# Performance work log

Hardware: AMD Instinct MI355X
Metric: run time of the kernel (lower is better)

The kernel has to match this reference:

```python
import jax, jax.numpy as jnp
import numpy as np

HEAD_DIM = 128
NUM_Q_HEADS = 32
NUM_KV_HEADS = 8
HIDDEN = HEAD_DIM * NUM_Q_HEADS  # 4096
ROPE_BASE = 10000.0


def setup_inputs() -> dict:
    key = jax.random.key(0)
    k1, k2, k3, k4, k5 = jax.random.split(key, 5)
    B, S = 1, 2048
    scale = 0.02  # keep activations sane given integer-valued x
    input_ids = jax.random.randint(k5, (B, S), 0, 100, dtype=jnp.int64) if jax.config.jax_enable_x64 else jax.random.randint(k5, (B, S), 0, 100, dtype=jnp.int32)
    position_ids = (jnp.arange(B * S).reshape(B, S) % S).astype(input_ids.dtype)
    Wq = jax.random.normal(k1, (HIDDEN, NUM_Q_HEADS * HEAD_DIM), dtype=jnp.float32) * scale
    Wk = jax.random.normal(k2, (HIDDEN, NUM_KV_HEADS * HEAD_DIM), dtype=jnp.float32) * scale
    Wv = jax.random.normal(k3, (HIDDEN, NUM_KV_HEADS * HEAD_DIM), dtype=jnp.float32) * scale
    Wo = jax.random.normal(k4, (NUM_Q_HEADS * HEAD_DIM, HIDDEN), dtype=jnp.float32) * scale
    return {"input_ids": input_ids, "position_ids": position_ids,
            "Wq": Wq, "Wk": Wk, "Wv": Wv, "Wo": Wo}


def _rotate_half(x):
    x1, x2 = jnp.split(x, 2, axis=-1)
    return jnp.concatenate([-x2, x1], axis=-1)


def _cos_sin(position_ids):
    # standard RoPE cos/sin, shape [B, S, 1, head_dim]
    inv_freq = 1.0 / (ROPE_BASE ** (jnp.arange(0, HEAD_DIM, 2, dtype=jnp.float32) / HEAD_DIM))
    ang = position_ids.astype(jnp.float32)[..., None] * inv_freq  # [B,S,d/2]
    cos = jnp.concatenate([jnp.cos(ang), jnp.cos(ang)], axis=-1)[:, :, None, :]
    sin = jnp.concatenate([jnp.sin(ang), jnp.sin(ang)], axis=-1)[:, :, None, :]
    return cos, sin


def reference(input_ids, position_ids, Wq, Wk, Wv, Wo):
    B, S = input_ids.shape
    # x = input_ids broadcast to hidden_size (as in the torch model)
    x = jnp.broadcast_to(input_ids[..., None].astype(jnp.float32), (B, S, HIDDEN))
    q = (x @ Wq).reshape(B, S, NUM_Q_HEADS, HEAD_DIM)
    k = (x @ Wk).reshape(B, S, NUM_KV_HEADS, HEAD_DIM)
    v = (x @ Wv).reshape(B, S, NUM_KV_HEADS, HEAD_DIM)
    cos, sin = _cos_sin(position_ids)
    q = q * cos + _rotate_half(q) * sin
    k = k * cos + _rotate_half(k) * sin
    # GQA: group q heads over kv heads
    G = NUM_Q_HEADS // NUM_KV_HEADS
    qg = q.reshape(B, S, NUM_KV_HEADS, G, HEAD_DIM)
    scores = jnp.einsum('bqhgd,bkhd->bhgqk', qg, k) / jnp.sqrt(jnp.float32(HEAD_DIM))
    causal = jnp.tril(jnp.ones((S, S), dtype=bool))  # [S_q, S_k]
    scores = jnp.where(causal, scores, -jnp.inf)
    attn = jax.nn.softmax(scores, axis=-1)
    out = jnp.einsum('bhgqk,bkhd->bqhgd', attn, v).reshape(B, S, NUM_Q_HEADS * HEAD_DIM)
    return out @ Wo
```

## Files before the change

### kernel.cpp

```cpp
#include <hip/hip_runtime.h>
#include <math.h>


#define HID 4096
#define NQH 32
#define NKVH 8
#define HD 128
#define CHQ 128
#define TS 64
#define RSQRT_HD 0.08838834764831845f
#define LOG2E    1.4426950408889634f

__device__ __forceinline__ void colsum_seq(const float* __restrict__ W,
                                           float* __restrict__ P,
                                           int nth4, int u) {
    const float4* b = reinterpret_cast<const float4*>(W);
    float ax = 0.f, ay = 0.f, az = 0.f, aw = 0.f;
#pragma unroll
    for (int k = 0; k < 32; k += 8) {
        float4 tt[8];
#pragma unroll
        for (int i = 0; i < 8; ++i) tt[i] = b[(size_t)(k + i) * nth4 + u];
#pragma unroll
        for (int i = 0; i < 8; i += 4) {
            ax += (tt[i].x + tt[i+1].x) + (tt[i+2].x + tt[i+3].x);
            ay += (tt[i].y + tt[i+1].y) + (tt[i+2].y + tt[i+3].y);
            az += (tt[i].z + tt[i+1].z) + (tt[i+2].z + tt[i+3].z);
            aw += (tt[i].w + tt[i+1].w) + (tt[i+2].w + tt[i+3].w);
        }
    }
    reinterpret_cast<float4*>(P)[u] = make_float4(ax, ay, az, aw);
}

__global__ __launch_bounds__(256) void k_part(
        const int* __restrict__ ids,
        const float* __restrict__ Wq, const float* __restrict__ Wk,
        const float* __restrict__ Wv,
        float* __restrict__ Pq, float* __restrict__ Pk, float* __restrict__ Pv,
        float* __restrict__ cp, double* __restrict__ Tc,
        double* __restrict__ Ts, int S) {
    int t = blockIdx.x;
    int tid = threadIdx.x;
    int nxb = S >> 8;
    int trigT = 64 * nxb;
    if (t < trigT) {
        int j = t / nxb, xb = t - j * nxb;
        int dlt = xb * 256 + tid;
        double f = (double)(float)(1.0 / pow(10000.0, (double)j / 64.0));
        double sv, cv;
        sincos((double)dlt * f, &sv, &cv);
        Tc[(size_t)j * S + dlt] = cv;
        Ts[(size_t)j * S + dlt] = sv;
        if (j == 0) cp[dlt] = (float)ids[dlt];
    } else if (t < trigT + 512) {
        colsum_seq(Wq, Pq, 512 * 256, (t - trigT) * 256 + tid);
    } else if (t < trigT + 640) {
        colsum_seq(Wk, Pk, 128 * 256, (t - trigT - 512) * 256 + tid);
    } else {
        colsum_seq(Wv, Pv, 128 * 256, (t - trigT - 640) * 256 + tid);
    }
}

__global__ __launch_bounds__(256) void k_red(
        const float* __restrict__ Pq, const float* __restrict__ Pk,
        const float* __restrict__ Pv, float* __restrict__ Sq,
        float* __restrict__ Sk, float* __restrict__ Sv) {
    int t = blockIdx.x;
    const float* P; float* Sd; int cols4, c4;
    if (t < 4)      { P = Pq; Sd = Sq; cols4 = NQH * HD / 4; c4 = t * 256 + threadIdx.x; }
    else if (t == 4){ P = Pk; Sd = Sk; cols4 = NKVH * HD / 4; c4 = threadIdx.x; }
    else            { P = Pv; Sd = Sv; cols4 = NKVH * HD / 4; c4 = threadIdx.x; }
    const float4* b = reinterpret_cast<const float4*>(P);
    float ax = 0.f, ay = 0.f, az = 0.f, aw = 0.f;
    for (int c = 0; c < CHQ; c += 16) {
        float4 tt[16];
#pragma unroll
        for (int i = 0; i < 16; ++i) tt[i] = b[(size_t)(c + i) * cols4 + c4];
#pragma unroll
        for (int i = 0; i < 16; i += 4) {
            ax += (tt[i].x + tt[i+1].x) + (tt[i+2].x + tt[i+3].x);
            ay += (tt[i].y + tt[i+1].y) + (tt[i+2].y + tt[i+3].y);
            az += (tt[i].z + tt[i+1].z) + (tt[i+2].z + tt[i+3].z);
            aw += (tt[i].w + tt[i+1].w) + (tt[i+2].w + tt[i+3].w);
        }
    }
    reinterpret_cast<float4*>(Sd)[c4] = make_float4(ax, ay, az, aw);
}

__global__ __launch_bounds__(256) void k_mid(
        const float* __restrict__ Sq, const float* __restrict__ Sk,
        const float* __restrict__ Sv, const float* __restrict__ Wo,
        const double* __restrict__ Tc, const double* __restrict__ Ts,
        float* __restrict__ Mp, float* __restrict__ D, int S) {
    int t = blockIdx.x;
    int tid = threadIdx.x;
    if (t < 512) {
        int sl = t & 3, x = (t >> 2) & 3, hg = t >> 4;
        int h = hg >> 2, dbase = hg * HD + sl * 32;
        int i4 = x * 256 + tid;
        const float4* b = reinterpret_cast<const float4*>(Wo);
        const float* sv = Sv + h * HD + sl * 32;
        float ax = 0.f, ay = 0.f, az = 0.f, aw = 0.f;
#pragma unroll
        for (int bb = 0; bb < 4; ++bb) {
            size_t p = (size_t)(dbase + bb * 8) * (HID / 4) + i4;
            float4 tt[8]; float ss[8];
#pragma unroll
            for (int i = 0; i < 8; ++i) { tt[i] = b[p + (size_t)i * (HID / 4)]; ss[i] = sv[bb * 8 + i]; }
#pragma unroll
            for (int i = 0; i < 8; ++i) {
                ax += ss[i] * tt[i].x; ay += ss[i] * tt[i].y;
                az += ss[i] * tt[i].z; aw += ss[i] * tt[i].w;
            }
        }
        reinterpret_cast<float4*>(Mp)[((size_t)sl * NQH + hg) * (HID / 4) + i4] =
            make_float4(ax, ay, az, aw);
    } else {
        __shared__ double p[64], q[64];
        int u = t - 512;
        int nxb = S >> 8;
        int hg = u / nxb, xb = u - hg * nxb, h = hg >> 2;
        if (tid < 64) {
            double a1 = Sq[hg * HD + tid], a2 = Sq[hg * HD + tid + 64];
            double b1 = Sk[h * HD + tid],  b2 = Sk[h * HD + tid + 64];
            p[tid] = a1 * b1 + a2 * b2;
            q[tid] = a2 * b1 - a1 * b2;
        }
        __syncthreads();
        int dlt = xb * 256 + tid;
        const double* tc = Tc + dlt;
        const double* ts = Ts + dlt;
        double acc = 0.0;
#pragma unroll 8
        for (int j = 0; j < 64; ++j)
            acc += p[j] * tc[(size_t)j * S] - q[j] * ts[(size_t)j * S];
        D[(size_t)hg * S + dlt] = (float)acc;
    }
}

__global__ __launch_bounds__(256) void k_alpha(
        const int* __restrict__ ids, const float* __restrict__ cp,
        const float* __restrict__ D, const float* __restrict__ Mp,
        float* __restrict__ M, float* __restrict__ A, int S) {
    int t = blockIdx.x;
    int tid = threadIdx.x;
    int nAlpha = (S / TS) * NQH;
    if (t >= nAlpha) {
        int u = t - nAlpha;
        const float4* mp = reinterpret_cast<const float4*>(Mp);
        float4* m4 = reinterpret_cast<float4*>(M);
        const int Q = NQH * HID / 4;
        for (int j = u * 256 + tid; j < Q; j += 16 * 256) {
            float4 a = mp[j], b = mp[j + Q], c = mp[j + 2 * Q], d = mp[j + 3 * Q];
            m4[j] = make_float4(a.x + b.x + c.x + d.x, a.y + b.y + c.y + d.y,
                                a.z + b.z + c.z + d.z, a.w + b.w + c.w + d.w);
        }
        return;
    }
    int tile = t >> 5;
    int hg = t & 31;
    int s0 = S - TS - tile * TS;
    int w = tid >> 6, lane = tid & 63;
    int sl = s0 + lane;
    float csl = (float)ids[sl] * (RSQRT_HD * LOG2E);
    const float* Drow = D + (size_t)hg * S + sl;

    int n = s0 + TS;
    int q4 = ((n + 15) >> 4) << 2;
    int k = w * q4;
    int k1 = (k + q4 < n) ? k + q4 : n;
    int lim = (k1 < s0 + 1) ? k1 : s0 + 1;

    float tm = -1e30f;
    float mz = csl * tm;
    float se = 0.f, sp = 0.f;

    for (; k + 8 <= lim; k += 8) {
        float4 cv0 = *reinterpret_cast<const float4*>(cp + k);
        float4 cv1 = *reinterpret_cast<const float4*>(cp + k + 4);
        float d0 = Drow[-k],     d1 = Drow[-(k+1)], d2 = Drow[-(k+2)], d3 = Drow[-(k+3)];
        float d4 = Drow[-(k+4)], d5 = Drow[-(k+5)], d6 = Drow[-(k+6)], d7 = Drow[-(k+7)];
        float t0 = cv0.x * d0, t1 = cv0.y * d1, t2 = cv0.z * d2, t3 = cv0.w * d3;
        float t4 = cv1.x * d4, t5 = cv1.y * d5, t6 = cv1.z * d6, t7 = cv1.w * d7;
        float m8 = fmaxf(fmaxf(fmaxf(t0, t1), fmaxf(t2, t3)),
                         fmaxf(fmaxf(t4, t5), fmaxf(t6, t7)));
        if (!__all(m8 <= tm)) {
            float ntm = fmaxf(tm, m8);
            float nmz = csl * ntm;
            float r = __builtin_amdgcn_exp2f(fminf(mz - nmz, 0.f));
            se *= r; sp *= r; tm = ntm; mz = nmz;
        }
        float e0 = __builtin_amdgcn_exp2f(fmaf(csl, t0, -mz));
        float e1 = __builtin_amdgcn_exp2f(fmaf(csl, t1, -mz));
        float e2 = __builtin_amdgcn_exp2f(fmaf(csl, t2, -mz));
        float e3 = __builtin_amdgcn_exp2f(fmaf(csl, t3, -mz));
        float e4 = __builtin_amdgcn_exp2f(fmaf(csl, t4, -mz));
        float e5 = __builtin_amdgcn_exp2f(fmaf(csl, t5, -mz));
        float e6 = __builtin_amdgcn_exp2f(fmaf(csl, t6, -mz));
        float e7 = __builtin_amdgcn_exp2f(fmaf(csl, t7, -mz));
        se += ((e0 + e1) + (e2 + e3)) + ((e4 + e5) + (e6 + e7));
        sp = fmaf(e0, cv0.x, sp); sp = fmaf(e1, cv0.y, sp);
        sp = fmaf(e2, cv0.z, sp); sp = fmaf(e3, cv0.w, sp);
        sp = fmaf(e4, cv1.x, sp); sp = fmaf(e5, cv1.y, sp);
        sp = fmaf(e6, cv1.z, sp); sp = fmaf(e7, cv1.w, sp);
    }
    for (; k + 4 <= lim; k += 4) {
        float4 cv = *reinterpret_cast<const float4*>(cp + k);
        float d0 = Drow[-k], d1 = Drow[-(k+1)], d2 = Drow[-(k+2)], d3 = Drow[-(k+3)];
        float t0 = cv.x * d0, t1 = cv.y * d1, t2 = cv.z * d2, t3 = cv.w * d3;
        float m4 = fmaxf(fmaxf(t0, t1), fmaxf(t2, t3));
        if (!__all(m4 <= tm)) {
            float ntm = fmaxf(tm, m4);
            float nmz = csl * ntm;
            float r = __builtin_amdgcn_exp2f(fminf(mz - nmz, 0.f));
            se *= r; sp *= r; tm = ntm; mz = nmz;
        }
        float e0 = __builtin_amdgcn_exp2f(fmaf(csl, t0, -mz));
        float e1 = __builtin_amdgcn_exp2f(fmaf(csl, t1, -mz));
        float e2 = __builtin_amdgcn_exp2f(fmaf(csl, t2, -mz));
        float e3 = __builtin_amdgcn_exp2f(fmaf(csl, t3, -mz));
        se += (e0 + e1) + (e2 + e3);
        sp = fmaf(e0, cv.x, sp); sp = fmaf(e1, cv.y, sp);
        sp = fmaf(e2, cv.z, sp); sp = fmaf(e3, cv.w, sp);
    }
    for (; k < k1; k += 4) {
        float4 cv = *reinterpret_cast<const float4*>(cp + k);
        float d0 = Drow[-k], d1 = Drow[-(k+1)], d2 = Drow[-(k+2)], d3 = Drow[-(k+3)];
        bool v0 = (k + 0 <= sl) && (k + 0 < k1);
        bool v1 = (k + 1 <= sl) && (k + 1 < k1);
        bool v2 = (k + 2 <= sl) && (k + 2 < k1);
        bool v3 = (k + 3 <= sl) && (k + 3 < k1);
        float t0 = v0 ? cv.x * d0 : -1e30f;
        float t1 = v1 ? cv.y * d1 : -1e30f;
        float t2 = v2 ? cv.z * d2 : -1e30f;
        float t3 = v3 ? cv.w * d3 : -1e30f;
        float m4 = fmaxf(fmaxf(t0, t1), fmaxf(t2, t3));
        if (!__all(m4 <= tm)) {
            float ntm = fmaxf(tm, m4);
            float nmz = csl * ntm;
            float r = __builtin_amdgcn_exp2f(fminf(mz - nmz, 0.f));
            se *= r; sp *= r; tm = ntm; mz = nmz;
        }
        float e0 = __builtin_amdgcn_exp2f(fmaf(csl, t0, -mz)); e0 = v0 ? e0 : 0.f;
        float e1 = __builtin_amdgcn_exp2f(fmaf(csl, t1, -mz)); e1 = v1 ? e1 : 0.f;
        float e2 = __builtin_amdgcn_exp2f(fmaf(csl, t2, -mz)); e2 = v2 ? e2 : 0.f;
        float e3 = __builtin_amdgcn_exp2f(fmaf(csl, t3, -mz)); e3 = v3 ? e3 : 0.f;
        se += (e0 + e1) + (e2 + e3);
        sp = fmaf(e0, cv.x, sp); sp = fmaf(e1, cv.y, sp);
        sp = fmaf(e2, cv.z, sp); sp = fmaf(e3, cv.w, sp);
    }

    __shared__ float lm[4][TS], ls[4][TS], lp[4][TS];
    lm[w][lane] = mz; ls[w][lane] = se; lp[w][lane] = sp;
    __syncthreads();
    if (tid < TS) {
        float m0 = lm[0][tid], m1 = lm[1][tid], m2 = lm[2][tid], m3 = lm[3][tid];
        float mm = fmaxf(fmaxf(m0, m1), fmaxf(m2, m3));
        float r0 = __builtin_amdgcn_exp2f(fminf(m0 - mm, 0.f));
        float r1 = __builtin_amdgcn_exp2f(fminf(m1 - mm, 0.f));
        float r2 = __builtin_amdgcn_exp2f(fminf(m2 - mm, 0.f));
        float r3 = __builtin_amdgcn_exp2f(fminf(m3 - mm, 0.f));
        float seT = ls[0][tid] * r0 + ls[1][tid] * r1 + ls[2][tid] * r2 + ls[3][tid] * r3;
        float spT = lp[0][tid] * r0 + lp[1][tid] * r1 + lp[2][tid] * r2 + lp[3][tid] * r3;
        A[(size_t)hg * S + s0 + tid] = spT / seT;
    }
}

__global__ void k_out(const float* __restrict__ A, const float* __restrict__ M,
                      float* __restrict__ out, int S) {
    __shared__ float a[512];
    int tid = threadIdx.x;
    int s0 = blockIdx.y * 16;
    for (int v = tid; v < 512; v += 256) {
        int hg = v >> 4, r = v & 15;
        a[r * NQH + hg] = A[(size_t)hg * S + s0 + r];
    }
    __syncthreads();
    int i = blockIdx.x * 256 + tid;
    float acc[16];
#pragma unroll
    for (int rr = 0; rr < 16; ++rr) acc[rr] = 0.f;
    for (int hg = 0; hg < NQH; ++hg) {
        float mv = M[(size_t)hg * HID + i];
#pragma unroll
        for (int rr = 0; rr < 16; ++rr) acc[rr] += a[rr * NQH + hg] * mv;
    }
#pragma unroll
    for (int rr = 0; rr < 16; ++rr)
        out[(size_t)(s0 + rr) * HID + i] = acc[rr];
}

extern "C" void kernel_launch(void* const* d_in, const int* in_sizes, int n_in,
                              void* d_out, int out_size, void* d_ws, size_t ws_size,
                              hipStream_t stream) {
    const int*   ids = (const int*)d_in[0];
    const float* Wq  = (const float*)d_in[2];
    const float* Wk  = (const float*)d_in[3];
    const float* Wv  = (const float*)d_in[4];
    const float* Wo  = (const float*)d_in[5];
    float* out = (float*)d_out;
    const int S = in_sizes[0];
    const int nxb = S >> 8;

    float* ws = (float*)d_ws;
    float* Pq = ws;
    float* Pk = Pq + (size_t)CHQ * NQH * HD;
    float* Pv = Pk + (size_t)CHQ * NKVH * HD;
    float* Mp = Pq;
    float* Sq = Pv + (size_t)CHQ * NKVH * HD;
    float* Sk = Sq + HID;
    float* Sv = Sk + NKVH * HD;
    float* D  = Sv + NKVH * HD;
    float* cp = D + (size_t)NQH * S;
    float* A  = cp + S;
    float* M  = A + (size_t)NQH * S;
    double* Tc = (double*)(M + (size_t)NQH * HID);
    double* Ts = Tc + (size_t)64 * S;

    k_part<<<64 * nxb + 512 + 128 + 128, 256, 0, stream>>>(
        ids, Wq, Wk, Wv, Pq, Pk, Pv, cp, Tc, Ts, S);
    k_red<<<6, 256, 0, stream>>>(Pq, Pk, Pv, Sq, Sk, Sv);
    k_mid<<<512 + NQH * nxb, 256, 0, stream>>>(Sq, Sk, Sv, Wo, Tc, Ts, Mp, D, S);
    k_alpha<<<(S / TS) * NQH + 16, 256, 0, stream>>>(ids, cp, D, Mp, M, A, S);
    k_out<<<dim3(HID / 256, S / 16), 256, 0, stream>>>(A, M, out, S);
}
```

Before: 85.01 us.

## Fold partial-sum reductions into consumers and cut kernel launches from five to four

Removes the tiny k_red kernel by having each D-table block and each Wo-projection block redundantly reduce the column partial sums it needs. The Wo projection now runs alongside the softmax/alpha blocks in one launch, and the final Mp partial reduction moves into k_out. Mp is aliased onto the Tc buffer, which is dead once k_dtab finishes. This saves launches and serialization points, at the cost of redundant reduction reads of Pq/Pk/Pv and four Mp loads per element in k_out.

Measured after the change: 89.71 us. +5.5%, slower.

```diff
diff --git a/kernel.cpp b/kernel.cpp
--- a/kernel.cpp
+++ b/kernel.cpp
@@ -61,104 +61,98 @@
     }
 }
 
-__global__ __launch_bounds__(256) void k_red(
+__global__ __launch_bounds__(256) void k_dtab(
         const float* __restrict__ Pq, const float* __restrict__ Pk,
-        const float* __restrict__ Pv, float* __restrict__ Sq,
-        float* __restrict__ Sk, float* __restrict__ Sv) {
-    int t = blockIdx.x;
-    const float* P; float* Sd; int cols4, c4;
-    if (t < 4)      { P = Pq; Sd = Sq; cols4 = NQH * HD / 4; c4 = t * 256 + threadIdx.x; }
-    else if (t == 4){ P = Pk; Sd = Sk; cols4 = NKVH * HD / 4; c4 = threadIdx.x; }
-    else            { P = Pv; Sd = Sv; cols4 = NKVH * HD / 4; c4 = threadIdx.x; }
-    const float4* b = reinterpret_cast<const float4*>(P);
-    float ax = 0.f, ay = 0.f, az = 0.f, aw = 0.f;
-    for (int c = 0; c < CHQ; c += 16) {
-        float4 tt[16];
-#pragma unroll
-        for (int i = 0; i < 16; ++i) tt[i] = b[(size_t)(c + i) * cols4 + c4];
-#pragma unroll
-        for (int i = 0; i < 16; i += 4) {
-            ax += (tt[i].x + tt[i+1].x) + (tt[i+2].x + tt[i+3].x);
-            ay += (tt[i].y + tt[i+1].y) + (tt[i+2].y + tt[i+3].y);
-            az += (tt[i].z + tt[i+1].z) + (tt[i+2].z + tt[i+3].z);
-            aw += (tt[i].w + tt[i+1].w) + (tt[i+2].w + tt[i+3].w);
-        }
-    }
-    reinterpret_cast<float4*>(Sd)[c4] = make_float4(ax, ay, az, aw);
-}
-
-__global__ __launch_bounds__(256) void k_mid(
-        const float* __restrict__ Sq, const float* __restrict__ Sk,
-        const float* __restrict__ Sv, const float* __restrict__ Wo,
         const double* __restrict__ Tc, const double* __restrict__ Ts,
-        float* __restrict__ Mp, float* __restrict__ D, int S) {
+        float* __restrict__ D, int S) {
+    __shared__ float sq[128], sk[128];
+    __shared__ double p[64], q[64];
+    int nxb = S >> 8;
+    int hg = blockIdx.x / nxb, xb = blockIdx.x - hg * nxb, h = hg >> 2;
+    int tid = threadIdx.x;
+    if (tid < 128) {
+        const float* base = Pq + hg * HD + tid;
+        float a = 0.f;
+#pragma unroll 16
+        for (int dep = 0; dep < CHQ; ++dep) a += base[(size_t)dep * 4096];
+        sq[tid] = a;
+    } else {
+        int d = tid - 128;
+        const float* base = Pk + h * HD + d;
+        float a = 0.f;
+#pragma unroll 16
+        for (int dep = 0; dep < CHQ; ++dep) a += base[(size_t)dep * 1024];
+        sk[d] = a;
+    }
+    __syncthreads();
+    if (tid < 64) {
+        double a1 = sq[tid], a2 = sq[tid + 64];
+        double b1 = sk[tid], b2 = sk[tid + 64];
+        p[tid] = a1 * b1 + a2 * b2;
+        q[tid] = a2 * b1 - a1 * b2;
+    }
+    __syncthreads();
+    int dlt = xb * 256 + tid;
+    const double* tc = Tc + dlt;
+    const double* ts = Ts + dlt;
+    double acc = 0.0;
+#pragma unroll 8
+    for (int j = 0; j < 64; ++j)
+        acc += p[j] * tc[(size_t)j * S] - q[j] * ts[(size_t)j * S];
+    D[(size_t)hg * S + dlt] = (float)acc;
+}
+
+__global__ __launch_bounds__(256) void k_fuse(
+        const int* __restrict__ ids, const float* __restrict__ cp,
+        const float* __restrict__ D, const float* __restrict__ Pv,
+        const float* __restrict__ Wo, float* __restrict__ Mp,
+        float* __restrict__ A, int S) {
     int t = blockIdx.x;
     int tid = threadIdx.x;
     if (t < 512) {
-        int sl = t & 3, x = (t >> 2) & 3, hg = t >> 4;
-        int h = hg >> 2, dbase = hg * HD + sl * 32;
+        __shared__ float part[8][32];
+        __shared__ float svs[32];
+        int sl = t & 3, x = (t >> 2) & 3, hg = t >> 4, h = hg >> 2;
+        {
+            int j = tid & 31, g = tid >> 5;
+            const float* base = Pv + (size_t)(g * 16) * 1024 + h * HD + sl * 32 + j;
+            float a = 0.f;
+#pragma unroll
+            for (int dep = 0; dep < 16; ++dep) a += base[(size_t)dep * 1024];
+            part[g][j] = a;
+        }
+        __syncthreads();
+        if (tid < 32) {
+            float a = 0.f;
+#pragma unroll
+            for (int g = 0; g < 8; ++g) a += part[g][tid];
+            svs[tid] = a;
+        }
+        __syncthreads();
+        int dbase = hg * HD + sl * 32;
         int i4 = x * 256 + tid;
         const float4* b = reinterpret_cast<const float4*>(Wo);
-        const float* sv = Sv + h * HD + sl * 32;
         float ax = 0.f, ay = 0.f, az = 0.f, aw = 0.f;
 #pragma unroll
         for (int bb = 0; bb < 4; ++bb) {
-            size_t p = (size_t)(dbase + bb * 8) * (HID / 4) + i4;
-            float4 tt[8]; float ss[8];
-#pragma unroll
-            for (int i = 0; i < 8; ++i) { tt[i] = b[p + (size_t)i * (HID / 4)]; ss[i] = sv[bb * 8 + i]; }
+            size_t pbase = (size_t)(dbase + bb * 8) * (HID / 4) + i4;
+            float4 tt[8];
+#pragma unroll
+            for (int i = 0; i < 8; ++i) tt[i] = b[pbase + (size_t)i * (HID / 4)];
 #pragma unroll
             for (int i = 0; i < 8; ++i) {
-                ax += ss[i] * tt[i].x; ay += ss[i] * tt[i].y;
-                az += ss[i] * tt[i].z; aw += ss[i] * tt[i].w;
+                float ss = svs[bb * 8 + i];
+                ax += ss * tt[i].x; ay += ss * tt[i].y;
+                az += ss * tt[i].z; aw += ss * tt[i].w;
             }
         }
         reinterpret_cast<float4*>(Mp)[((size_t)sl * NQH + hg) * (HID / 4) + i4] =
             make_float4(ax, ay, az, aw);
-    } else {
-        __shared__ double p[64], q[64];
-        int u = t - 512;
-        int nxb = S >> 8;
-        int hg = u / nxb, xb = u - hg * nxb, h = hg >> 2;
-        if (tid < 64) {
-            double a1 = Sq[hg * HD + tid], a2 = Sq[hg * HD + tid + 64];
-            double b1 = Sk[h * HD + tid],  b2 = Sk[h * HD + tid + 64];
-            p[tid] = a1 * b1 + a2 * b2;
-            q[tid] = a2 * b1 - a1 * b2;
-        }
-        __syncthreads();
-        int dlt = xb * 256 + tid;
-        const double* tc = Tc + dlt;
-        const double* ts = Ts + dlt;
-        double acc = 0.0;
-#pragma unroll 8
-        for (int j = 0; j < 64; ++j)
-            acc += p[j] * tc[(size_t)j * S] - q[j] * ts[(size_t)j * S];
-        D[(size_t)hg * S + dlt] = (float)acc;
-    }
-}
-
-__global__ __launch_bounds__(256) void k_alpha(
-        const int* __restrict__ ids, const float* __restrict__ cp,
-        const float* __restrict__ D, const float* __restrict__ Mp,
-        float* __restrict__ M, float* __restrict__ A, int S) {
-    int t = blockIdx.x;
-    int tid = threadIdx.x;
-    int nAlpha = (S / TS) * NQH;
-    if (t >= nAlpha) {
-        int u = t - nAlpha;
-        const float4* mp = reinterpret_cast<const float4*>(Mp);
-        float4* m4 = reinterpret_cast<float4*>(M);
-        const int Q = NQH * HID / 4;
-        for (int j = u * 256 + tid; j < Q; j += 16 * 256) {
-            float4 a = mp[j], b = mp[j + Q], c = mp[j + 2 * Q], d = mp[j + 3 * Q];
-            m4[j] = make_float4(a.x + b.x + c.x + d.x, a.y + b.y + c.y + d.y,
-                                a.z + b.z + c.z + d.z, a.w + b.w + c.w + d.w);
-        }
         return;
     }
-    int tile = t >> 5;
-    int hg = t & 31;
+    int u = t - 512;
+    int tile = u >> 5;
+    int hg = u & 31;
     int s0 = S - TS - tile * TS;
     int w = tid >> 6, lane = tid & 63;
     int sl = s0 + lane;
@@ -266,7 +260,7 @@
     }
 }
 
-__global__ void k_out(const float* __restrict__ A, const float* __restrict__ M,
+__global__ void k_out(const float* __restrict__ A, const float* __restrict__ Mp,
                       float* __restrict__ out, int S) {
     __shared__ float a[512];
     int tid = threadIdx.x;
@@ -277,11 +271,13 @@
     }
     __syncthreads();
     int i = blockIdx.x * 256 + tid;
+    const int Q = NQH * HID;
     float acc[16];
 #pragma unroll
     for (int rr = 0; rr < 16; ++rr) acc[rr] = 0.f;
     for (int hg = 0; hg < NQH; ++hg) {
-        float mv = M[(size_t)hg * HID + i];
+        size_t base = (size_t)hg * HID + i;
+        float mv = (Mp[base] + Mp[base + Q]) + (Mp[base + 2 * Q] + Mp[base + 3 * Q]);
 #pragma unroll
         for (int rr = 0; rr < 16; ++rr) acc[rr] += a[rr * NQH + hg] * mv;
     }
@@ -306,21 +302,16 @@
     float* Pq = ws;
     float* Pk = Pq + (size_t)CHQ * NQH * HD;
     float* Pv = Pk + (size_t)CHQ * NKVH * HD;
-    float* Mp = Pq;
-    float* Sq = Pv + (size_t)CHQ * NKVH * HD;
-    float* Sk = Sq + HID;
-    float* Sv = Sk + NKVH * HD;
-    float* D  = Sv + NKVH * HD;
+    float* D  = Pv + (size_t)CHQ * NKVH * HD;
     float* cp = D + (size_t)NQH * S;
     float* A  = cp + S;
-    float* M  = A + (size_t)NQH * S;
-    double* Tc = (double*)(M + (size_t)NQH * HID);
+    double* Tc = (double*)(A + (size_t)NQH * S);
     double* Ts = Tc + (size_t)64 * S;
+    float* Mp = (float*)Tc;
 
     k_part<<<64 * nxb + 512 + 128 + 128, 256, 0, stream>>>(
         ids, Wq, Wk, Wv, Pq, Pk, Pv, cp, Tc, Ts, S);
-    k_red<<<6, 256, 0, stream>>>(Pq, Pk, Pv, Sq, Sk, Sv);
-    k_mid<<<512 + NQH * nxb, 256, 0, stream>>>(Sq, Sk, Sv, Wo, Tc, Ts, Mp, D, S);
-    k_alpha<<<(S / TS) * NQH + 16, 256, 0, stream>>>(ids, cp, D, Mp, M, A, S);
-    k_out<<<dim3(HID / 256, S / 16), 256, 0, stream>>>(A, M, out, S);
-}
+    k_dtab<<<NQH * nxb, 256, 0, stream>>>(Pq, Pk, Tc, Ts, D, S);
+    k_fuse<<<512 + (S / TS) * NQH, 256, 0, stream>>>(ids, cp, D, Pv, Wo, Mp, A, S);
+    k_out<<<dim3(HID / 256, S / 16), 256, 0, stream>>>(A, Mp, out, S);
+}
```
